# Performance work log

Hardware: AMD Instinct MI355X
Metric: run time of the kernel (lower is better)

## Reference

```python
import jax, jax.numpy as jnp
import numpy as np

DIM = 768
HEADS = 12
DIM_HEAD = 64
INNER = HEADS * DIM_HEAD  # 768
B, N = 8, 1024
SCALE = DIM_HEAD ** -0.5


def setup_inputs() -> dict:
    key = jax.random.key(0)
    ks = jax.random.split(key, 8)
    std = 0.02
    x = jax.random.normal(ks[0], (B, N, DIM), dtype=jnp.float32)
    W_q = jax.random.normal(ks[1], (DIM, INNER), dtype=jnp.float32) * std
    W_kv = jax.random.normal(ks[2], (DIM, 2 * INNER), dtype=jnp.float32) * std
    mix_pre = jax.random.normal(ks[3], (HEADS, HEADS), dtype=jnp.float32)
    mix_post = jax.random.normal(ks[4], (HEADS, HEADS), dtype=jnp.float32)
    W_out = jax.random.normal(ks[5], (INNER, DIM), dtype=jnp.float32) * std
    b_out = jnp.zeros((DIM,), dtype=jnp.float32)
    return {"x": x, "W_q": W_q, "W_kv": W_kv, "mix_pre": mix_pre,
            "mix_post": mix_post, "W_out": W_out, "b_out": b_out}


def reference(x, W_q, W_kv, mix_pre, mix_post, W_out, b_out):
    b, n, _ = x.shape
    # projections (context == x since no cross-attn context given)
    q = x @ W_q                                   # (b, n, inner)
    kv = x @ W_kv                                 # (b, n, 2*inner)
    k, v = jnp.split(kv, 2, axis=-1)
    # (b, n, h*d) -> (b, h, n, d)
    split_heads = lambda t: t.reshape(b, n, HEADS, DIM_HEAD).transpose(0, 2, 1, 3)
    q, k, v = split_heads(q), split_heads(k), split_heads(v)
    dots = jnp.einsum('bhid,bhjd->bhij', q, k) * SCALE
    dots = jnp.einsum('bhij,hg->bgij', dots, mix_pre)    # pre-softmax talking heads
    attn = jax.nn.softmax(dots, axis=-1)
    attn = jnp.einsum('bhij,hg->bgij', attn, mix_post)   # post-softmax talking heads
    out = jnp.einsum('bhij,bhjd->bhid', attn, v)         # (b, h, n, d)
    out = out.transpose(0, 2, 1, 3).reshape(b, n, INNER)
    return out @ W_out + b_out
```

## Files before the change

kernel.cpp:

```cpp
#include <hip/hip_runtime.h>
#include <hip/hip_bf16.h>

typedef __attribute__((ext_vector_type(8))) short short8_t;
typedef __attribute__((ext_vector_type(8))) unsigned short ushort8_t;
typedef __attribute__((ext_vector_type(4))) float f32x4;

#define SCALE 0.125f

__device__ __forceinline__ unsigned short f32_to_bf16_rne(float f) {
  unsigned int u = __float_as_uint(f);
  unsigned int r = 0x7FFFu + ((u >> 16) & 1u);
  return (unsigned short)((u + r) >> 16);
}

__device__ __forceinline__ int swz(int i) { return (i + (i >> 2)) & 3; }

__global__ __launch_bounds__(256) void cast_x_kernel(const float4* __restrict__ in,
                                                     ushort4* __restrict__ out, int n4) {
  int i = blockIdx.x * 256 + threadIdx.x;
  if (i < n4) {
    float4 v = in[i];
    ushort4 o;
    o.x = f32_to_bf16_rne(v.x); o.y = f32_to_bf16_rne(v.y);
    o.z = f32_to_bf16_rne(v.z); o.w = f32_to_bf16_rne(v.w);
    out[i] = o;
  }
}

__global__ __launch_bounds__(256) void transpose_cast_kernel(const float* __restrict__ in,
                                                             unsigned short* __restrict__ out,
                                                             int R, int C) {
  __shared__ float tile[32][33];
  int c0 = blockIdx.x * 32, r0 = blockIdx.y * 32;
  int tx = threadIdx.x & 31, ty = threadIdx.x >> 5;
  #pragma unroll
  for (int i = ty; i < 32; i += 8)
    tile[i][tx] = in[(long)(r0 + i) * C + c0 + tx];
  __syncthreads();
  #pragma unroll
  for (int i = ty; i < 32; i += 8)
    out[(long)(c0 + i) * R + r0 + tx] = f32_to_bf16_rne(tile[tx][i]);
}

__global__ __launch_bounds__(256) void transpose_v_kernel(const unsigned short* __restrict__ KV,
                                                          unsigned short* __restrict__ Vt) {
  __shared__ unsigned short tile[64][72];
  const int j0 = blockIdx.x * 64, h = blockIdx.y, b = blockIdx.z;
  const int tid = threadIdx.x;
  for (int c = tid; c < 512; c += 256) {
    int j = c >> 3, dp = (c & 7) * 8;
    *(ushort8_t*)&tile[j][dp] =
        *(const ushort8_t*)&KV[(long)(b * 1024 + j0 + j) * 1536 + 768 + h * 64 + dp];
  }
  __syncthreads();
  for (int c = tid; c < 512; c += 256) {
    int d = c >> 3, jp = (c & 7) * 8;
    ushort8_t v;
    #pragma unroll
    for (int t = 0; t < 8; t++) v[t] = tile[jp + t][d];
    int jg = j0 + jp;
    int jt_ = jg >> 5;
    int u = (jg >> 3) & 3;
    *(ushort8_t*)&Vt[((long)(b * 12 + h) * 64 + d) * 1024 + (jt_ << 5) + ((u ^ swz(d)) << 3)] = v;
  }
}

template <int BM, int BN, bool OUT_F32, bool BIAS, bool SUM2>
__global__ __launch_bounds__(256) void gemm_nt(const unsigned short* __restrict__ A,
                                               const unsigned short* __restrict__ A2, int lda,
                                               const unsigned short* __restrict__ B, int ldb,
                                               void* __restrict__ Cv, int ldc,
                                               const float* __restrict__ bias,
                                               int M, int N, int K) {
  constexpr int BK = 32;
  constexpr int LDT = BK + 8;
  __shared__ unsigned short As[BM][LDT];
  __shared__ unsigned short Bs[BN][LDT];
  const int m0 = blockIdx.y * BM;
  const int n0 = blockIdx.x * BN;
  const int tid = threadIdx.x;
  const int lane = tid & 63;
  const int w = tid >> 6;
  constexpr int WM = BM / 2, WN = BN / 2;
  constexpr int FM = WM / 16, FN = WN / 16;
  const int wr = w >> 1, wc = w & 1;

  f32x4 acc[FM][FN];
  #pragma unroll
  for (int a = 0; a < FM; a++)
    #pragma unroll
    for (int b2 = 0; b2 < FN; b2++) acc[a][b2] = (f32x4){0.f, 0.f, 0.f, 0.f};

  const int rl = lane & 15;
  const int kq = (lane >> 4) * 8;

  for (int k0 = 0; k0 < K; k0 += BK) {
    __syncthreads();
    for (int c = tid; c < BM * (BK / 8); c += 256) {
      int row = c >> 2, kp = (c & 3) * 8;
      ushort8_t v = *(const ushort8_t*)&A[(long)(m0 + row) * lda + k0 + kp];
      if (SUM2) {
        ushort8_t v2 = *(const ushort8_t*)&A2[(long)(m0 + row) * lda + k0 + kp];
        #pragma unroll
        for (int x = 0; x < 8; ++x)
          v[x] = f32_to_bf16_rne(__uint_as_float((unsigned)v[x] << 16) +
                                 __uint_as_float((unsigned)v2[x] << 16));
      }
      *(ushort8_t*)&As[row][kp] = v;
    }
    for (int c = tid; c < BN * (BK / 8); c += 256) {
      int row = c >> 2, kp = (c & 3) * 8;
      *(ushort8_t*)&Bs[row][kp] = *(const ushort8_t*)&B[(long)(n0 + row) * ldb + k0 + kp];
    }
    __syncthreads();
    short8_t af[FM], bfr[FN];
    #pragma unroll
    for (int fm = 0; fm < FM; fm++) af[fm] = *(const short8_t*)&As[wr * WM + fm * 16 + rl][kq];
    #pragma unroll
    for (int fn = 0; fn < FN; fn++) bfr[fn] = *(const short8_t*)&Bs[wc * WN + fn * 16 + rl][kq];
    #pragma unroll
    for (int fm = 0; fm < FM; fm++)
      #pragma unroll
      for (int fn = 0; fn < FN; fn++)
        acc[fm][fn] = __builtin_amdgcn_mfma_f32_16x16x32_bf16(af[fm], bfr[fn], acc[fm][fn], 0, 0, 0);
  }

  const int rq4 = (lane >> 4) * 4;
  #pragma unroll
  for (int fm = 0; fm < FM; fm++)
    #pragma unroll
    for (int fn = 0; fn < FN; fn++)
      #pragma unroll
      for (int j = 0; j < 4; j++) {
        int row = m0 + wr * WM + fm * 16 + rq4 + j;
        int col = n0 + wc * WN + fn * 16 + rl;
        float v = acc[fm][fn][j];
        if (BIAS) v += bias[col];
        if (OUT_F32)
          ((float*)Cv)[(long)row * ldc + col] = v;
        else
          ((unsigned short*)Cv)[(long)row * ldc + col] = f32_to_bf16_rne(v);
      }
}

__global__ __launch_bounds__(256, 1) void qk_mix_exp_kernel(
    const unsigned short* __restrict__ Qb, const unsigned short* __restrict__ KVb,
    const float* __restrict__ mix_pre,
    unsigned short* __restrict__ Eo, float* __restrict__ Lpart, int b_base) {
  __shared__ unsigned short Ebuf[24576];
  __shared__ float mpre_s[144];
  const int jt = blockIdx.x, it = blockIdx.y, z = blockIdx.z;
  const int b = b_base + z;
  const int tid = threadIdx.x, lane = tid & 63, w = tid >> 6;
  const int r15 = lane & 15, q = lane >> 4;
  if (tid < 144) mpre_s[tid] = mix_pre[tid] * SCALE;
  __syncthreads();
  const int i0 = it * 64, j0 = jt * 32;

  const long qrow  = (long)(b * 1024 + i0 + w * 16 + r15) * 768 + q * 8;
  const long krow0 = (long)(b * 1024 + j0 + r15) * 1536 + q * 8;
  const long krow1 = (long)(b * 1024 + j0 + 16 + r15) * 1536 + q * 8;

  float macc[12][2][4];
  #pragma unroll
  for (int g = 0; g < 12; ++g)
    #pragma unroll
    for (int nf = 0; nf < 2; ++nf)
      #pragma unroll
      for (int e = 0; e < 4; ++e) macc[g][nf][e] = 0.f;

  for (int h = 0; h < 12; ++h) {
    const int kb = h * 64;
    short8_t a0  = *(const short8_t*)&Qb[qrow + kb];
    short8_t a1  = *(const short8_t*)&Qb[qrow + kb + 32];
    short8_t b00 = *(const short8_t*)&KVb[krow0 + kb];
    short8_t b01 = *(const short8_t*)&KVb[krow0 + kb + 32];
    short8_t b10 = *(const short8_t*)&KVb[krow1 + kb];
    short8_t b11 = *(const short8_t*)&KVb[krow1 + kb + 32];
    f32x4 h0 = {0.f, 0.f, 0.f, 0.f}, h1 = {0.f, 0.f, 0.f, 0.f};
    h0 = __builtin_amdgcn_mfma_f32_16x16x32_bf16(a0, b00, h0, 0, 0, 0);
    h0 = __builtin_amdgcn_mfma_f32_16x16x32_bf16(a1, b01, h0, 0, 0, 0);
    h1 = __builtin_amdgcn_mfma_f32_16x16x32_bf16(a0, b10, h1, 0, 0, 0);
    h1 = __builtin_amdgcn_mfma_f32_16x16x32_bf16(a1, b11, h1, 0, 0, 0);
    #pragma unroll
    for (int g = 0; g < 12; ++g) {
      const float wgt = mpre_s[h * 12 + g];
      #pragma unroll
      for (int e = 0; e < 4; ++e) {
        macc[g][0][e] += wgt * h0[e];
        macc[g][1][e] += wgt * h1[e];
      }
    }
  }

  #pragma unroll
  for (int g = 0; g < 12; ++g)
    #pragma unroll
    for (int nf = 0; nf < 2; ++nf)
      #pragma unroll
      for (int e = 0; e < 4; ++e) macc[g][nf][e] = __expf(macc[g][nf][e]);

  float ls[12][4];
  #pragma unroll
  for (int g = 0; g < 12; ++g)
    #pragma unroll
    for (int e = 0; e < 4; ++e) ls[g][e] = macc[g][0][e] + macc[g][1][e];
  #pragma unroll
  for (int off = 1; off < 16; off <<= 1)
    #pragma unroll
    for (int g = 0; g < 12; ++g)
      #pragma unroll
      for (int e = 0; e < 4; ++e) ls[g][e] += __shfl_xor(ls[g][e], off);
  #pragma unroll
  for (int g = 0; g < 12; ++g)
    if (r15 == g) {
      #pragma unroll
      for (int e = 0; e < 4; ++e)
        Lpart[((long)(z * 32 + jt) * 12 + g) * 1024 + i0 + w * 16 + q * 4 + e] = ls[g][e];
    }

  #pragma unroll
  for (int g = 0; g < 12; ++g)
    #pragma unroll
    for (int nf = 0; nf < 2; ++nf)
      #pragma unroll
      for (int e = 0; e < 4; ++e) {
        const int r = q * 4 + e;
        const int jsl = nf * 2 + (r15 >> 3);
        Ebuf[(w * 12 + g) * 512 + r * 32 + ((jsl ^ swz(r)) << 3) + (r15 & 7)] =
            f32_to_bf16_rne(macc[g][nf][e]);
      }
  __syncthreads();
  const long cb = ((long)((z * 32 + jt) * 16 + it)) * 24576;
  #pragma unroll
  for (int u = 0; u < 12; ++u)
    *(ushort8_t*)&Eo[cb + (u * 256 + tid) * 8] = *(const ushort8_t*)&Ebuf[(u * 256 + tid) * 8];
}

__global__ __launch_bounds__(256) void lsum_kernel(const float* __restrict__ Lpart,
                                                   float* __restrict__ invl, int nb) {
  int id = blockIdx.x * 256 + threadIdx.x;
  if (id >= nb * 12288) return;
  int z = id / 12288, r = id - z * 12288;
  float s = 0.f;
  #pragma unroll 4
  for (int jt = 0; jt < 32; ++jt) s += Lpart[((long)(z * 32 + jt)) * 12288 + r];
  invl[id] = 1.f / s;
}

__global__ __launch_bounds__(256, 1) void pv2_kernel(
    const unsigned short* __restrict__ E, const unsigned short* __restrict__ Vt,
    const float* __restrict__ invl, const float* __restrict__ mix_post,
    unsigned short* __restrict__ AOp0, unsigned short* __restrict__ AOp1, int b_base) {
  __shared__ unsigned short Ebuf[6144];
  __shared__ unsigned short Vbuf[24576];
  __shared__ unsigned short Pbuf[6144];
  const int it = blockIdx.x, jh = blockIdx.y, zc = blockIdx.z;
  const int b = b_base + zc;
  const int tid = threadIdx.x, lane = tid & 63, w = tid >> 6;
  const int r15 = lane & 15, q = lane >> 4;
  const int i_loc = tid & 15, jslot = (tid >> 4) & 3;

  float W2[3][12];
  #pragma unroll
  for (int g = 0; g < 12; ++g) {
    float il = invl[(zc * 12 + g) * 1024 + it * 16 + i_loc];
    #pragma unroll
    for (int r = 0; r < 3; ++r) W2[r][g] = mix_post[g * 12 + w * 3 + r] * il;
  }

  f32x4 acc[3][4];
  #pragma unroll
  for (int gl = 0; gl < 3; ++gl)
    #pragma unroll
    for (int df = 0; df < 4; ++df) acc[gl][df] = (f32x4){0.f, 0.f, 0.f, 0.f};

  const long vbase = (long)(b * 12) * 64 * 1024;
  ushort8_t ereg[3], vreg[12];
  auto loadE = [&](int jt) {
    const long cbs = ((long)((zc * 32 + jt) * 16 + (it >> 2))) * 24576 + (it & 3) * 6144;
    #pragma unroll
    for (int u = 0; u < 3; ++u)
      ereg[u] = *(const ushort8_t*)&E[cbs + (u * 256 + tid) * 8];
  };
  auto loadV = [&](int jt) {
    #pragma unroll
    for (int u = 0; u < 12; ++u) {
      int unit = u * 256 + tid;
      vreg[u] = *(const ushort8_t*)&Vt[vbase + (long)(unit >> 2) * 1024 + jt * 32 +
                                       ((unit & 3) << 3)];
    }
  };
  const int jt0 = jh * 16;
  loadE(jt0);
  loadV(jt0);

  for (int t = 0; t < 16; ++t) {
    __syncthreads();
    #pragma unroll
    for (int u = 0; u < 3; ++u) *(ushort8_t*)&Ebuf[(u * 256 + tid) * 8] = ereg[u];
    #pragma unroll
    for (int u = 0; u < 12; ++u) *(ushort8_t*)&Vbuf[(u * 256 + tid) * 8] = vreg[u];
    __syncthreads();
    if (t < 15) { loadE(jt0 + t + 1); loadV(jt0 + t + 1); }

    float p[3][8];
    #pragma unroll
    for (int r = 0; r < 3; ++r)
      #pragma unroll
      for (int jj = 0; jj < 8; ++jj) p[r][jj] = 0.f;
    const int esl = (jslot ^ swz(i_loc)) << 3;
    #pragma unroll
    for (int g = 0; g < 12; ++g) {
      ushort8_t ev = *(const ushort8_t*)&Ebuf[g * 512 + i_loc * 32 + esl];
      #pragma unroll
      for (int jj = 0; jj < 8; ++jj) {
        float ef = __uint_as_float((unsigned)ev[jj] << 16);
        #pragma unroll
        for (int r = 0; r < 3; ++r) p[r][jj] += W2[r][g] * ef;
      }
    }
    #pragma unroll
    for (int r = 0; r < 3; ++r) {
      ushort8_t pv;
      #pragma unroll
      for (int jj = 0; jj < 8; ++jj) pv[jj] = f32_to_bf16_rne(p[r][jj]);
      *(ushort8_t*)&Pbuf[(w * 3 + r) * 512 + i_loc * 32 + esl] = pv;
    }
    __syncthreads();

    #pragma unroll
    for (int gl = 0; gl < 3; ++gl) {
      const int g2 = w * 3 + gl;
      short8_t af = *(const short8_t*)&Pbuf[g2 * 512 + r15 * 32 + ((q ^ swz(r15)) << 3)];
      #pragma unroll
      for (int df = 0; df < 4; ++df) {
        short8_t bf = *(const short8_t*)&Vbuf[(g2 * 64 + df * 16 + r15) * 32 +
                                              ((q ^ swz(r15)) << 3)];
        acc[gl][df] = __builtin_amdgcn_mfma_f32_16x16x32_bf16(af, bf, acc[gl][df], 0, 0, 0);
      }
    }
  }

  unsigned short* AOp = jh ? AOp1 : AOp0;
  #pragma unroll
  for (int gl = 0; gl < 3; ++gl) {
    const int g2 = w * 3 + gl;
    #pragma unroll
    for (int df = 0; df < 4; ++df)
      #pragma unroll
      for (int e = 0; e < 4; ++e) {
        int row = it * 16 + q * 4 + e;
        int col = g2 * 64 + df * 16 + r15;
        AOp[(long)(b * 1024 + row) * 768 + col] = f32_to_bf16_rne(acc[gl][df][e]);
      }
  }
}

extern "C" void kernel_launch(void* const* d_in, const int* in_sizes, int n_in,
                              void* d_out, int out_size, void* d_ws, size_t ws_size,
                              hipStream_t stream) {
  const float* x        = (const float*)d_in[0];
  const float* W_q      = (const float*)d_in[1];
  const float* W_kv     = (const float*)d_in[2];
  const float* mix_pre  = (const float*)d_in[3];
  const float* mix_post = (const float*)d_in[4];
  const float* W_out    = (const float*)d_in[5];
  const float* b_out    = (const float*)d_in[6];
  float* out = (float*)d_out;

  char* p = (char*)d_ws;
  auto alloc = [&](size_t bytes) { char* r = p; p += (bytes + 255) & ~(size_t)255; return r; };
  unsigned short* xb    = (unsigned short*)alloc(8192ull * 768 * 2);
  unsigned short* WqT   = (unsigned short*)alloc(768ull * 768 * 2);
  unsigned short* WkvT  = (unsigned short*)alloc(1536ull * 768 * 2);
  unsigned short* WoutT = (unsigned short*)alloc(768ull * 768 * 2);
  unsigned short* Qb    = (unsigned short*)alloc(8192ull * 768 * 2);
  unsigned short* KVb   = (unsigned short*)alloc(8192ull * 1536 * 2);
  unsigned short* Vt    = (unsigned short*)alloc(8ull * 12 * 64 * 1024 * 2);
  unsigned short* AOp0  = (unsigned short*)alloc(8192ull * 768 * 2);
  unsigned short* AOp1  = (unsigned short*)alloc(8192ull * 768 * 2);

  const int nz = (ws_size >= 322000000ull) ? 8 : (ws_size >= 211000000ull) ? 4 : 2;
  unsigned short* E     = (unsigned short*)alloc((size_t)nz * 32 * 16 * 24576 * 2);
  float*          Lpart = (float*)alloc((size_t)nz * 32 * 12 * 1024 * 4);
  float*          invl  = (float*)alloc((size_t)nz * 12 * 1024 * 4);

  cast_x_kernel<<<6144, 256, 0, stream>>>((const float4*)x, (ushort4*)xb, 8192 * 768 / 4);
  transpose_cast_kernel<<<dim3(24, 24), 256, 0, stream>>>(W_q, WqT, 768, 768);
  transpose_cast_kernel<<<dim3(48, 24), 256, 0, stream>>>(W_kv, WkvT, 768, 1536);
  transpose_cast_kernel<<<dim3(24, 24), 256, 0, stream>>>(W_out, WoutT, 768, 768);

  gemm_nt<128, 128, false, false, false><<<dim3(6, 64), 256, 0, stream>>>(
      xb, nullptr, 768, WqT, 768, Qb, 768, nullptr, 8192, 768, 768);
  gemm_nt<128, 128, false, false, false><<<dim3(12, 64), 256, 0, stream>>>(
      xb, nullptr, 768, WkvT, 768, KVb, 1536, nullptr, 8192, 1536, 768);

  transpose_v_kernel<<<dim3(16, 12, 8), 256, 0, stream>>>(KVb, Vt);

  for (int b0 = 0; b0 < 8; b0 += nz) {
    qk_mix_exp_kernel<<<dim3(32, 16, nz), 256, 0, stream>>>(Qb, KVb, mix_pre, E, Lpart, b0);
    lsum_kernel<<<nz * 48, 256, 0, stream>>>(Lpart, invl, nz);
    pv2_kernel<<<dim3(64, 2, nz), 256, 0, stream>>>(E, Vt, invl, mix_post, AOp0, AOp1, b0);
  }

  gemm_nt<128, 128, true, true, true><<<dim3(6, 64), 256, 0, stream>>>(
      AOp0, AOp1, 768, WoutT, 768, out, 768, b_out, 8192, 768, 768);
}
```

Measured before the change: 457.3 us.

## Restructure QK-mix-exp kernel to stage per-head dots in LDS before mixing

The QK/mix/exp kernel now has each wave compute one 16x16 tile of per-head dot products, store them as bf16 in shared memory, then remap threads so each owns 4 columns of one row to do the 12x12 head mix, exp and row-sum. The tile shrinks to 32x32, which doubles the grid, and the old 96-float per-thread accumulator goes away, cutting register pressure. Writes to E go straight to global memory without an extra LDS staging copy. The cost is rounding the pre-mix dots to bf16, which adds precision loss before the exp, plus an LDS round trip and a barrier.

```diff
diff --git a/kernel.cpp b/kernel.cpp
--- a/kernel.cpp
+++ b/kernel.cpp
@@ -147,94 +147,72 @@
     const unsigned short* __restrict__ Qb, const unsigned short* __restrict__ KVb,
     const float* __restrict__ mix_pre,
     unsigned short* __restrict__ Eo, float* __restrict__ Lpart, int b_base) {
-  __shared__ unsigned short Ebuf[24576];
+  __shared__ unsigned short Dbuf[12 * 32 * 44];
   __shared__ float mpre_s[144];
-  const int jt = blockIdx.x, it = blockIdx.y, z = blockIdx.z;
-  const int b = b_base + z;
+  const int jt = blockIdx.x, it2 = blockIdx.y, zc = blockIdx.z;
+  const int b = b_base + zc;
   const int tid = threadIdx.x, lane = tid & 63, w = tid >> 6;
   const int r15 = lane & 15, q = lane >> 4;
   if (tid < 144) mpre_s[tid] = mix_pre[tid] * SCALE;
-  __syncthreads();
-  const int i0 = it * 64, j0 = jt * 32;
-
-  const long qrow  = (long)(b * 1024 + i0 + w * 16 + r15) * 768 + q * 8;
-  const long krow0 = (long)(b * 1024 + j0 + r15) * 1536 + q * 8;
-  const long krow1 = (long)(b * 1024 + j0 + 16 + r15) * 1536 + q * 8;
-
-  float macc[12][2][4];
-  #pragma unroll
-  for (int g = 0; g < 12; ++g)
-    #pragma unroll
-    for (int nf = 0; nf < 2; ++nf)
-      #pragma unroll
-      for (int e = 0; e < 4; ++e) macc[g][nf][e] = 0.f;
-
+
+  const int isel = w >> 1, jsel = w & 1;
+  const long qrow = (long)(b * 1024 + it2 * 32 + isel * 16 + r15) * 768 + q * 8;
+  const long krow = (long)(b * 1024 + jt * 32 + jsel * 16 + r15) * 1536 + q * 8;
+  const int jcol = jsel * 16 + r15;
   for (int h = 0; h < 12; ++h) {
     const int kb = h * 64;
-    short8_t a0  = *(const short8_t*)&Qb[qrow + kb];
-    short8_t a1  = *(const short8_t*)&Qb[qrow + kb + 32];
-    short8_t b00 = *(const short8_t*)&KVb[krow0 + kb];
-    short8_t b01 = *(const short8_t*)&KVb[krow0 + kb + 32];
-    short8_t b10 = *(const short8_t*)&KVb[krow1 + kb];
-    short8_t b11 = *(const short8_t*)&KVb[krow1 + kb + 32];
-    f32x4 h0 = {0.f, 0.f, 0.f, 0.f}, h1 = {0.f, 0.f, 0.f, 0.f};
-    h0 = __builtin_amdgcn_mfma_f32_16x16x32_bf16(a0, b00, h0, 0, 0, 0);
-    h0 = __builtin_amdgcn_mfma_f32_16x16x32_bf16(a1, b01, h0, 0, 0, 0);
-    h1 = __builtin_amdgcn_mfma_f32_16x16x32_bf16(a0, b10, h1, 0, 0, 0);
-    h1 = __builtin_amdgcn_mfma_f32_16x16x32_bf16(a1, b11, h1, 0, 0, 0);
-    #pragma unroll
-    for (int g = 0; g < 12; ++g) {
+    short8_t a0 = *(const short8_t*)&Qb[qrow + kb];
+    short8_t a1 = *(const short8_t*)&Qb[qrow + kb + 32];
+    short8_t b0 = *(const short8_t*)&KVb[krow + kb];
+    short8_t b1 = *(const short8_t*)&KVb[krow + kb + 32];
+    f32x4 h0 = {0.f, 0.f, 0.f, 0.f};
+    h0 = __builtin_amdgcn_mfma_f32_16x16x32_bf16(a0, b0, h0, 0, 0, 0);
+    h0 = __builtin_amdgcn_mfma_f32_16x16x32_bf16(a1, b1, h0, 0, 0, 0);
+    #pragma unroll
+    for (int e = 0; e < 4; ++e) {
+      int il = isel * 16 + q * 4 + e;
+      Dbuf[h * 1408 + il * 44 + jcol] = f32_to_bf16_rne(h0[e]);
+    }
+  }
+  __syncthreads();
+
+  const int i_loc = tid >> 3;
+  const int jg = tid & 7;
+  const int r = i_loc & 15;
+  const long chunkbase = ((long)((zc * 32 + jt) * 64) + it2 * 2 + (i_loc >> 4)) * 6144;
+  const int eslot = r * 32 + ((((jg >> 1) ^ swz(r))) << 3) + (jg & 1) * 4;
+
+  float dvf[12][4];
+  #pragma unroll
+  for (int h = 0; h < 12; ++h) {
+    ushort4 dv = *(const ushort4*)&Dbuf[h * 1408 + i_loc * 44 + jg * 4];
+    dvf[h][0] = __uint_as_float((unsigned)dv.x << 16);
+    dvf[h][1] = __uint_as_float((unsigned)dv.y << 16);
+    dvf[h][2] = __uint_as_float((unsigned)dv.z << 16);
+    dvf[h][3] = __uint_as_float((unsigned)dv.w << 16);
+  }
+
+  #pragma unroll
+  for (int g = 0; g < 12; ++g) {
+    float a0 = 0.f, a1 = 0.f, a2 = 0.f, a3 = 0.f;
+    #pragma unroll
+    for (int h = 0; h < 12; ++h) {
       const float wgt = mpre_s[h * 12 + g];
-      #pragma unroll
-      for (int e = 0; e < 4; ++e) {
-        macc[g][0][e] += wgt * h0[e];
-        macc[g][1][e] += wgt * h1[e];
-      }
-    }
-  }
-
-  #pragma unroll
-  for (int g = 0; g < 12; ++g)
-    #pragma unroll
-    for (int nf = 0; nf < 2; ++nf)
-      #pragma unroll
-      for (int e = 0; e < 4; ++e) macc[g][nf][e] = __expf(macc[g][nf][e]);
-
-  float ls[12][4];
-  #pragma unroll
-  for (int g = 0; g < 12; ++g)
-    #pragma unroll
-    for (int e = 0; e < 4; ++e) ls[g][e] = macc[g][0][e] + macc[g][1][e];
-  #pragma unroll
-  for (int off = 1; off < 16; off <<= 1)
-    #pragma unroll
-    for (int g = 0; g < 12; ++g)
-      #pragma unroll
-      for (int e = 0; e < 4; ++e) ls[g][e] += __shfl_xor(ls[g][e], off);
-  #pragma unroll
-  for (int g = 0; g < 12; ++g)
-    if (r15 == g) {
-      #pragma unroll
-      for (int e = 0; e < 4; ++e)
-        Lpart[((long)(z * 32 + jt) * 12 + g) * 1024 + i0 + w * 16 + q * 4 + e] = ls[g][e];
-    }
-
-  #pragma unroll
-  for (int g = 0; g < 12; ++g)
-    #pragma unroll
-    for (int nf = 0; nf < 2; ++nf)
-      #pragma unroll
-      for (int e = 0; e < 4; ++e) {
-        const int r = q * 4 + e;
-        const int jsl = nf * 2 + (r15 >> 3);
-        Ebuf[(w * 12 + g) * 512 + r * 32 + ((jsl ^ swz(r)) << 3) + (r15 & 7)] =
-            f32_to_bf16_rne(macc[g][nf][e]);
-      }
-  __syncthreads();
-  const long cb = ((long)((z * 32 + jt) * 16 + it)) * 24576;
-  #pragma unroll
-  for (int u = 0; u < 12; ++u)
-    *(ushort8_t*)&Eo[cb + (u * 256 + tid) * 8] = *(const ushort8_t*)&Ebuf[(u * 256 + tid) * 8];
+      a0 += wgt * dvf[h][0]; a1 += wgt * dvf[h][1];
+      a2 += wgt * dvf[h][2]; a3 += wgt * dvf[h][3];
+    }
+    a0 = __expf(a0); a1 = __expf(a1); a2 = __expf(a2); a3 = __expf(a3);
+    float s = a0 + a1 + a2 + a3;
+    s += __shfl_xor(s, 1);
+    s += __shfl_xor(s, 2);
+    s += __shfl_xor(s, 4);
+    if (jg == (g & 7))
+      Lpart[((long)(zc * 32 + jt) * 12 + g) * 1024 + it2 * 32 + i_loc] = s;
+    ushort4 ev;
+    ev.x = f32_to_bf16_rne(a0); ev.y = f32_to_bf16_rne(a1);
+    ev.z = f32_to_bf16_rne(a2); ev.w = f32_to_bf16_rne(a3);
+    *(ushort4*)&Eo[chunkbase + g * 512 + eslot] = ev;
+  }
 }
 
 __global__ __launch_bounds__(256) void lsum_kernel(const float* __restrict__ Lpart,
@@ -399,7 +377,7 @@
   transpose_v_kernel<<<dim3(16, 12, 8), 256, 0, stream>>>(KVb, Vt);
 
   for (int b0 = 0; b0 < 8; b0 += nz) {
-    qk_mix_exp_kernel<<<dim3(32, 16, nz), 256, 0, stream>>>(Qb, KVb, mix_pre, E, Lpart, b0);
+    qk_mix_exp_kernel<<<dim3(32, 32, nz), 256, 0, stream>>>(Qb, KVb, mix_pre, E, Lpart, b0);
     lsum_kernel<<<nz * 48, 256, 0, stream>>>(Lpart, invl, nz);
     pv2_kernel<<<dim3(64, 2, nz), 256, 0, stream>>>(E, Vt, invl, mix_post, AOp0, AOp1, b0);
   }
```

Measured after the change: 487.7 us. +6.7%, slower.
